# Kernel tuning notes

Hardware: AMD Instinct MI355X
Metric: run time of the kernel (lower is better)

Reference implementation:

```python
import jax, jax.numpy as jnp
import numpy as np

N_NODES = 50000
N_RAND_EDGES = 1_600_000
IN_F = 512
HID = 64
HEADS = 8
N_CLASSES = 20
SLOPE = 0.2  # LeakyReLU negative slope


def setup_inputs() -> dict:
    key = jax.random.key(0)
    ks = jax.random.split(key, 6)
    x = jax.random.normal(ks[0], (N_NODES, IN_F), dtype=jnp.float32)
    er = jax.random.randint(ks[1], (2, N_RAND_EDGES), 0, N_NODES)
    loops = jnp.tile(jnp.arange(N_NODES), (2, 1))  # self-loops so every row of adj is nonzero
    edge_index = jnp.concatenate([er, loops], axis=1)  # [2, E]
    # Learned parameters (per SpGraphAttentionLayer: weight [in,out], alpha [1,2*out] -> stored flat)
    W1 = jax.random.normal(ks[2], (HEADS, IN_F, HID), dtype=jnp.float32) * 0.05
    a1 = jax.random.normal(ks[3], (HEADS, 2 * HID), dtype=jnp.float32) * 0.1
    W2 = jax.random.normal(ks[4], (HEADS * HID, N_CLASSES), dtype=jnp.float32) * 0.05
    a2 = jax.random.normal(ks[5], (2 * N_CLASSES,), dtype=jnp.float32) * 0.1
    return {"x": x, "W1": W1, "a1": a1, "W2": W2, "a2": a2, "edge_index": edge_index}


def _gat_layer(x, W, a, e0, e1, n):
    # h = x @ weight; edge score = alpha . [h[src], h[dst]] computed as two per-node dots
    h = x @ W  # [N, F_out]
    f = W.shape[1]
    s_src = h @ a[:f]   # [N]
    s_dst = h @ a[f:]   # [N]
    edge_e = jnp.exp(jax.nn.leaky_relu(s_src[e0] + s_dst[e1], SLOPE))  # [E]
    rowsum = jax.ops.segment_sum(edge_e, e0, num_segments=n)  # spmm(adj_e, ones)
    agg = jax.ops.segment_sum(edge_e[:, None] * h[e1], e0, num_segments=n)  # spmm(adj_e, h)
    return agg / rowsum[:, None]


def reference(x, W1, a1, W2, a2, edge_index):
    n = x.shape[0]
    e0, e1 = edge_index[0], edge_index[1]
    # layer 1: per-head GAT, elu, concat along features (dropout is identity in eval)
    heads = [jax.nn.elu(_gat_layer(x, W1[i], a1[i], e0, e1, n)) for i in range(W1.shape[0])]
    hcat = jnp.concatenate(heads, axis=1)  # [N, HEADS*HID]
    out = jax.nn.elu(_gat_layer(hcat, W2, a2, e0, e1, n))  # [N, C]
    return out
```

## Files before the change

kernel.cpp:

```cpp
#include <hip/hip_runtime.h>
#include <hip/hip_fp16.h>
#include <math.h>

#define SLOPE 0.2f

typedef short bf16x8 __attribute__((ext_vector_type(8)));
typedef float f32x4  __attribute__((ext_vector_type(4)));

static __device__ __forceinline__ float elu_f(float x){ return x > 0.f ? x : (__expf(x) - 1.f); }
static __device__ __forceinline__ float lrelu(float t){ return t > 0.f ? t : SLOPE*t; }
static __device__ __forceinline__ unsigned short f2bf_rne(float f){
    unsigned int u = __float_as_uint(f);
    unsigned int r = (u + 0x7FFFu + ((u >> 16) & 1u)) >> 16;
    return (unsigned short)r;
}
static __device__ __forceinline__ float bf2f(unsigned short h){ return __uint_as_float(((unsigned int)h) << 16); }

#define ASYNC_COPY16(gp, lp) \
    __builtin_amdgcn_global_load_lds((const __attribute__((address_space(1))) void*)(gp), \
                                     (__attribute__((address_space(3))) void*)(lp), 16, 0, 0)

__global__ void __launch_bounds__(256) hist_sliced_kernel(const int* __restrict__ e0, int E, int n,
                                                          int* __restrict__ cnt){
    const int s = blockIdx.x & 7;
    const int c = blockIdx.x >> 3;
    const int K = gridDim.x >> 3;
    const int lo = (int)((long)s*n >> 3), hi = (int)((long)(s+1)*n >> 3);
    const int i0 = (int)((long)c*E/K), i1 = (int)((long)(c+1)*E/K);
    for (int i = i0 + threadIdx.x; i < i1; i += 256){
        int j = e0[i];
        if (j >= lo && j < hi) atomicAdd(&cnt[j], 1);
    }
}

__global__ void __launch_bounds__(1024) scan_kernel(const int* __restrict__ cnt, int n,
                                                    int* __restrict__ row_ptr, int* __restrict__ cursor){
    __shared__ int wtot[16];
    __shared__ int carry_sh;
    if (threadIdx.x == 0) carry_sh = 0;
    __syncthreads();
    const int lane = threadIdx.x & 63, wid = threadIdx.x >> 6;
    const int nch = (n + 1023) >> 10;
    for (int c = 0; c < nch; ++c){
        int i = (c << 10) + threadIdx.x;
        int v = (i < n) ? cnt[i] : 0;
        int val = v;
        #pragma unroll
        for (int off = 1; off < 64; off <<= 1){
            int t = __shfl_up(val, off, 64);
            if (lane >= off) val += t;
        }
        if (lane == 63) wtot[wid] = val;
        __syncthreads();
        int tot = 0, wexcl = 0;
        #pragma unroll
        for (int w = 0; w < 16; ++w){ int t = wtot[w]; tot += t; if (w < wid) wexcl += t; }
        int excl = carry_sh + wexcl + (val - v);
        if (i < n){ row_ptr[i] = excl; cursor[i] = excl; }
        __syncthreads();
        if (threadIdx.x == 0) carry_sh += tot;
        __syncthreads();
    }
    if (threadIdx.x == 0) row_ptr[n] = carry_sh;
}

__global__ void __launch_bounds__(256) scatter_sliced_kernel(const int* __restrict__ e0, const int* __restrict__ e1,
                                                             int E, int n,
                                                             int* __restrict__ cursor, int* __restrict__ sidx){
    const int s = blockIdx.x & 7;
    const int c = blockIdx.x >> 3;
    const int K = gridDim.x >> 3;
    const int lo = (int)((long)s*n >> 3), hi = (int)((long)(s+1)*n >> 3);
    const int i0 = (int)((long)c*E/K), i1 = (int)((long)(c+1)*E/K);
    for (int i = i0 + threadIdx.x; i < i1; i += 256){
        int j = e0[i];
        if (j >= lo && j < hi){
            int p = atomicAdd(&cursor[j], 1);
            sidx[p] = e1[i];
        }
    }
}

__global__ void __launch_bounds__(256) split_x_kernel(const float* __restrict__ x,
                                                      unsigned short* __restrict__ xhi,
                                                      unsigned short* __restrict__ xlo, int total4){
    int i = blockIdx.x*256 + threadIdx.x;
    if (i >= total4) return;
    float4 v = ((const float4*)x)[i];
    ushort4 h, l;
    h.x = f2bf_rne(v.x); l.x = f2bf_rne(v.x - bf2f(h.x));
    h.y = f2bf_rne(v.y); l.y = f2bf_rne(v.y - bf2f(h.y));
    h.z = f2bf_rne(v.z); l.z = f2bf_rne(v.z - bf2f(h.z));
    h.w = f2bf_rne(v.w); l.w = f2bf_rne(v.w - bf2f(h.w));
    ((ushort4*)xhi)[i] = h;
    ((ushort4*)xlo)[i] = l;
}

__global__ void __launch_bounds__(256) prep_w_kernel(const float* __restrict__ W1,
                                                     unsigned short* __restrict__ wThi,
                                                     unsigned short* __restrict__ wTlo){
    int idx = blockIdx.x*256 + threadIdx.x;
    int head = idx >> 15, rem = idx & 32767;
    int c = rem >> 9, k = rem & 511;
    float f = W1[((size_t)head << 15) + k*64 + c];
    unsigned short h = f2bf_rne(f);
    wThi[idx] = h;
    wTlo[idx] = f2bf_rne(f - bf2f(h));
}

__global__ void __launch_bounds__(256) gemm1_mfma_kernel(const unsigned short* __restrict__ xhi,
                                                         const unsigned short* __restrict__ xlo,
                                                         const unsigned short* __restrict__ wThi,
                                                         const unsigned short* __restrict__ wTlo,
                                                         const float* __restrict__ a1,
                                                         __half* __restrict__ h_g,
                                                         float* __restrict__ ssrc, float* __restrict__ sdst,
                                                         int n, int nwg){
    __shared__ unsigned short lds[16384];
    const int bid = blockIdx.x;
    const int xcd = bid & 7, jj = bid >> 3;
    const int q = nwg >> 3, r = nwg & 7;
    const int logical = (xcd < r ? xcd*(q+1) : r*(q+1) + (xcd-r)*q) + jj;
    const int rowtile = logical >> 2, ct = logical & 3;
    const int row0 = rowtile*128, col0 = ct*128;
    const int w = threadIdx.x >> 6, lane = threadIdx.x & 63;
    const int wm = w >> 1, wn = w & 1;
    const int lr = lane & 15, lk = lane >> 4;
    f32x4 acc[4][4] = {};
    const unsigned short* sbase[8];
    unsigned int soff[8];
    #pragma unroll
    for (int i = 0; i < 8; ++i){
        unsigned int off = w*8192u + i*1024u + lane*16u;
        unsigned int arr = off >> 13, within = off & 8191u;
        unsigned int rrow = within >> 6, kel = (within & 63u) >> 1;
        const unsigned short* g;
        size_t gidx;
        if (arr == 0)      { g = xhi;  gidx = (size_t)(row0 + rrow)*512 + kel; }
        else if (arr == 1) { g = xlo;  gidx = (size_t)(row0 + rrow)*512 + kel; }
        else if (arr == 2) { g = wThi; gidx = (size_t)(col0 + rrow)*512 + kel; }
        else               { g = wTlo; gidx = (size_t)(col0 + rrow)*512 + kel; }
        sbase[i] = g + gidx;
        soff[i] = (w*8192u + i*1024u);
    }
    const unsigned short* Ahi = lds;
    const unsigned short* Alo = lds + 4096;
    const unsigned short* Bhi = lds + 8192;
    const unsigned short* Blo = lds + 12288;
    for (int k0 = 0; k0 < 512; k0 += 32){
        #pragma unroll
        for (int i = 0; i < 8; ++i)
            ASYNC_COPY16(sbase[i] + k0, (char*)lds + soff[i]);
        __syncthreads();
        bf16x8 a_h[4], a_l[4], b_h[4], b_l[4];
        #pragma unroll
        for (int mi = 0; mi < 4; ++mi){
            int rowl = wm*64 + mi*16 + lr;
            a_h[mi] = *(const bf16x8*)(Ahi + rowl*32 + lk*8);
            a_l[mi] = *(const bf16x8*)(Alo + rowl*32 + lk*8);
        }
        #pragma unroll
        for (int ni = 0; ni < 4; ++ni){
            int coll = wn*64 + ni*16 + lr;
            b_h[ni] = *(const bf16x8*)(Bhi + coll*32 + lk*8);
            b_l[ni] = *(const bf16x8*)(Blo + coll*32 + lk*8);
        }
        #pragma unroll
        for (int mi = 0; mi < 4; ++mi)
            #pragma unroll
            for (int ni = 0; ni < 4; ++ni){
                f32x4& A = acc[mi][ni];
                A = __builtin_amdgcn_mfma_f32_16x16x32_bf16(a_h[mi], b_h[ni], A, 0, 0, 0);
                A = __builtin_amdgcn_mfma_f32_16x16x32_bf16(a_h[mi], b_l[ni], A, 0, 0, 0);
                A = __builtin_amdgcn_mfma_f32_16x16x32_bf16(a_l[mi], b_h[ni], A, 0, 0, 0);
            }
        __syncthreads();
    }
    const int head = ct*2 + wn;
    float as_[4], ad_[4];
    #pragma unroll
    for (int ni = 0; ni < 4; ++ni){
        as_[ni] = a1[(size_t)head*128 + ni*16 + lr];
        ad_[ni] = a1[(size_t)head*128 + 64 + ni*16 + lr];
    }
    #pragma unroll
    for (int mi = 0; mi < 4; ++mi){
        #pragma unroll
        for (int reg = 0; reg < 4; ++reg){
            float s = 0.f, d = 0.f;
            #pragma unroll
            for (int ni = 0; ni < 4; ++ni){
                float v = acc[mi][ni][reg];
                s += v*as_[ni]; d += v*ad_[ni];
            }
            s += __shfl_xor(s, 1); d += __shfl_xor(d, 1);
            s += __shfl_xor(s, 2); d += __shfl_xor(d, 2);
            s += __shfl_xor(s, 4); d += __shfl_xor(d, 4);
            s += __shfl_xor(s, 8); d += __shfl_xor(d, 8);
            const int node = row0 + wm*64 + mi*16 + lk*4 + reg;
            if (node < n){
                #pragma unroll
                for (int ni = 0; ni < 4; ++ni)
                    h_g[(size_t)node*512 + head*64 + ni*16 + lr] = __float2half(acc[mi][ni][reg]);
                if (lr == 0){
                    ssrc[(size_t)node*8 + head] = s;
                    sdst[(size_t)node*8 + head] = d;
                }
            }
        }
    }
}

__global__ void __launch_bounds__(256) agg1_kernel(const __half* __restrict__ h_g, const float* __restrict__ ssrc,
                                                   const float* __restrict__ sdst,
                                                   const int* __restrict__ row_ptr, const int* __restrict__ sidx,
                                                   __half* __restrict__ hcat, int n){
    const int w = threadIdx.x >> 6, lane = threadIdx.x & 63;
    const int node = blockIdx.x*4 + w;
    if (node >= n) return;
    const int r0 = row_ptr[node], r1 = row_ptr[node+1];
    const int h = lane >> 3;
    const float ssh = ssrc[(size_t)node*8 + h];
    float acc[8] = {};
    float wsum = 0.f;
    int e = r0;
    for (; e + 3 < r1; e += 4){
        int j0 = sidx[e], j1 = sidx[e+1], j2 = sidx[e+2], j3 = sidx[e+3];
        uint4 g0 = *(const uint4*)(h_g + (size_t)j0*512 + lane*8);
        uint4 g1 = *(const uint4*)(h_g + (size_t)j1*512 + lane*8);
        uint4 g2 = *(const uint4*)(h_g + (size_t)j2*512 + lane*8);
        uint4 g3 = *(const uint4*)(h_g + (size_t)j3*512 + lane*8);
        float s0 = sdst[(size_t)j0*8 + h], s1 = sdst[(size_t)j1*8 + h];
        float s2 = sdst[(size_t)j2*8 + h], s3 = sdst[(size_t)j3*8 + h];
        float w0 = __expf(lrelu(ssh + s0));
        float w1 = __expf(lrelu(ssh + s1));
        float w2 = __expf(lrelu(ssh + s2));
        float w3 = __expf(lrelu(ssh + s3));
        const unsigned int* u0 = &g0.x; const unsigned int* u1 = &g1.x;
        const unsigned int* u2 = &g2.x; const unsigned int* u3 = &g3.x;
        #pragma unroll
        for (int q = 0; q < 4; ++q){
            float2 f0 = __half22float2(*(const __half2*)&u0[q]);
            float2 f1 = __half22float2(*(const __half2*)&u1[q]);
            float2 f2 = __half22float2(*(const __half2*)&u2[q]);
            float2 f3 = __half22float2(*(const __half2*)&u3[q]);
            acc[2*q]   += w0*f0.x + w1*f1.x + w2*f2.x + w3*f3.x;
            acc[2*q+1] += w0*f0.y + w1*f1.y + w2*f2.y + w3*f3.y;
        }
        wsum += (w0 + w1) + (w2 + w3);
    }
    for (; e < r1; ++e){
        int j = sidx[e];
        uint4 g = *(const uint4*)(h_g + (size_t)j*512 + lane*8);
        float wg = __expf(lrelu(ssh + sdst[(size_t)j*8 + h]));
        const unsigned int* u = &g.x;
        #pragma unroll
        for (int q = 0; q < 4; ++q){
            float2 f = __half22float2(*(const __half2*)&u[q]);
            acc[2*q]   += wg*f.x;
            acc[2*q+1] += wg*f.y;
        }
        wsum += wg;
    }
    float inv = 1.f / wsum;
    union { uint4 u; __half hv[8]; } pk;
    #pragma unroll
    for (int q = 0; q < 8; ++q) pk.hv[q] = __float2half(elu_f(acc[q]*inv));
    *(uint4*)(hcat + (size_t)node*512 + lane*8) = pk.u;
}

__global__ void __launch_bounds__(256) gemm2_kernel(const __half* __restrict__ hcat, const float* __restrict__ W2,
                                                    const float* __restrict__ a2,
                                                    float* __restrict__ h2, float* __restrict__ ssrc,
                                                    float* __restrict__ sdst, int n){
    __shared__ float As[16][257];
    __shared__ float Ws[16][20];
    const int tid = threadIdx.x;
    const int node = blockIdx.x*256 + tid;
    float acc[20] = {};
    for (int k0 = 0; k0 < 512; k0 += 16){
        uint4 u0 = {0,0,0,0}, u1 = {0,0,0,0};
        if (node < n){
            const __half* src = hcat + (size_t)node*512 + k0;
            u0 = *(const uint4*)src;
            u1 = *(const uint4*)(src + 8);
        }
        const unsigned int* ua = &u0.x;
        const unsigned int* ub = &u1.x;
        #pragma unroll
        for (int q = 0; q < 4; ++q){
            float2 f = __half22float2(*(const __half2*)&ua[q]);
            As[2*q][tid] = f.x; As[2*q+1][tid] = f.y;
            float2 g = __half22float2(*(const __half2*)&ub[q]);
            As[8+2*q][tid] = g.x; As[8+2*q+1][tid] = g.y;
        }
        for (int q = tid; q < 320; q += 256){
            int kr = q/20, cc = q%20;
            Ws[kr][cc] = W2[(size_t)(k0 + kr)*20 + cc];
        }
        __syncthreads();
        #pragma unroll
        for (int kk = 0; kk < 16; ++kk){
            float a = As[kk][tid];
            #pragma unroll
            for (int cc = 0; cc < 20; ++cc) acc[cc] += a*Ws[kk][cc];
        }
        __syncthreads();
    }
    if (node < n){
        float s0 = 0.f, s1 = 0.f;
        #pragma unroll
        for (int cc = 0; cc < 20; ++cc){
            h2[(size_t)node*20 + cc] = acc[cc];
            s0 += acc[cc]*a2[cc];
            s1 += acc[cc]*a2[20 + cc];
        }
        ssrc[node] = s0; sdst[node] = s1;
    }
}

__global__ void __launch_bounds__(256) agg2_kernel(const float* __restrict__ h2, const float* __restrict__ ssrc,
                                                   const float* __restrict__ sdstv,
                                                   const int* __restrict__ row_ptr, const int* __restrict__ sidx,
                                                   float* __restrict__ out, int n){
    const int w = threadIdx.x >> 6, lane = threadIdx.x & 63;
    const int node = blockIdx.x*4 + w;
    if (node >= n) return;
    const int r0 = row_ptr[node], r1 = row_ptr[node+1];
    const float ss = ssrc[node];
    const bool act = lane < 20;
    float acc = 0.f, wsum = 0.f;
    int e = r0;
    for (; e + 3 < r1; e += 4){
        int j0 = sidx[e], j1 = sidx[e+1], j2 = sidx[e+2], j3 = sidx[e+3];
        float v0 = act ? h2[(size_t)j0*20 + lane] : 0.f;
        float v1 = act ? h2[(size_t)j1*20 + lane] : 0.f;
        float v2 = act ? h2[(size_t)j2*20 + lane] : 0.f;
        float v3 = act ? h2[(size_t)j3*20 + lane] : 0.f;
        float s0 = sdstv[j0], s1 = sdstv[j1], s2 = sdstv[j2], s3 = sdstv[j3];
        float w0 = __expf(lrelu(ss + s0));
        float w1 = __expf(lrelu(ss + s1));
        float w2 = __expf(lrelu(ss + s2));
        float w3 = __expf(lrelu(ss + s3));
        acc += w0*v0 + w1*v1 + w2*v2 + w3*v3;
        wsum += (w0 + w1) + (w2 + w3);
    }
    for (; e < r1; ++e){
        int j = sidx[e];
        float v = act ? h2[(size_t)j*20 + lane] : 0.f;
        float wg = __expf(lrelu(ss + sdstv[j]));
        acc += wg*v; wsum += wg;
    }
    if (act) out[(size_t)node*20 + lane] = elu_f(acc / wsum);
}

extern "C" void kernel_launch(void* const* d_in, const int* in_sizes, int n_in,
                              void* d_out, int out_size, void* d_ws, size_t ws_size,
                              hipStream_t stream){
    const float* x  = (const float*)d_in[0];
    const float* W1 = (const float*)d_in[1];
    const float* a1 = (const float*)d_in[2];
    const float* W2 = (const float*)d_in[3];
    const float* a2 = (const float*)d_in[4];
    const int*   ei = (const int*)d_in[5];
    const int n = in_sizes[0] / 512;
    const int E = in_sizes[5] / 2;
    const int* e0 = ei;
    const int* e1 = ei + E;

    char* p = (char*)d_ws;
    auto alloc = [&](size_t bytes)->char*{ char* r = p; p += (bytes + 255) & ~(size_t)255; return r; };
    unsigned short* xhi  = (unsigned short*)alloc((size_t)n*512*2);
    unsigned short* xlo  = (unsigned short*)alloc((size_t)n*512*2);
    __half*         h_g  = (__half*)        alloc((size_t)n*512*2);
    unsigned short* wThi = (unsigned short*)alloc((size_t)8*64*512*2);
    unsigned short* wTlo = (unsigned short*)alloc((size_t)8*64*512*2);
    float* ssrc1   = (float*)alloc((size_t)n*8*4);
    float* sdst1   = (float*)alloc((size_t)n*8*4);
    int*   cnt     = (int*)  alloc((size_t)n*4);
    int*   row_ptr = (int*)  alloc(((size_t)n + 1)*4);
    int*   cursor  = (int*)  alloc((size_t)n*4);
    int*   sidx    = (int*)  alloc((size_t)E*4);
    __half* hcat  = (__half*)xhi;
    float*  h2    = (float*)xlo;
    float*  ssrc2 = h2 + (size_t)n*20;
    float*  sdst2 = ssrc2 + n;

    hipMemsetAsync(cnt, 0, (size_t)n*4, stream);
    const int KCH = 192;
    hist_sliced_kernel   <<<KCH*8, 256, 0, stream>>>(e0, E, n, cnt);
    scan_kernel          <<<1, 1024, 0, stream>>>(cnt, n, row_ptr, cursor);
    scatter_sliced_kernel<<<KCH*8, 256, 0, stream>>>(e0, e1, E, n, cursor, sidx);

    const int total4 = n*512/4;
    split_x_kernel<<<(total4 + 255)/256, 256, 0, stream>>>(x, xhi, xlo, total4);
    prep_w_kernel <<<1024, 256, 0, stream>>>(W1, wThi, wTlo);

    const int mb = (n + 127)/128;
    const int nwg = mb*4;
    gemm1_mfma_kernel<<<nwg, 256, 0, stream>>>(xhi, xlo, wThi, wTlo, a1, h_g, ssrc1, sdst1, n, nwg);
    agg1_kernel      <<<(n + 3)/4, 256, 0, stream>>>(h_g, ssrc1, sdst1, row_ptr, sidx, hcat, n);

    const int nb256 = (n + 255)/256;
    gemm2_kernel<<<nb256, 256, 0, stream>>>(hcat, W2, a2, h2, ssrc2, sdst2, n);
    agg2_kernel <<<(n + 3)/4, 256, 0, stream>>>(h2, ssrc2, sdst2, row_ptr, sidx, (float*)d_out, n);
}
```

Baseline: 869.8 us.

## Bucket CSR neighbors by source-node range and parallelize the prefix scan

Each row's neighbor list is now grouped into buckets of 2048 source nodes by building per-(row, bucket) counters, so the aggregation gathers in agg1 and agg2 sweep through h_g in a rough, coherent order. The goal is better cache locality for the random feature gathers. The single-block serial scan is replaced by a three-kernel parallel reduce, small-scan and apply scan over the larger counter array. The CSR build now runs after gemm1, with its buffers placed inside the freed xlo workspace. In exchange, the counter array grows to n*25 entries, which adds memset, scan and atomic traffic.

```diff
diff --git a/kernel.cpp b/kernel.cpp
--- a/kernel.cpp
+++ b/kernel.cpp
@@ -3,6 +3,7 @@
 #include <math.h>
 
 #define SLOPE 0.2f
+#define SSHIFT 11
 
 typedef short bf16x8 __attribute__((ext_vector_type(8)));
 typedef float f32x4  __attribute__((ext_vector_type(4)));
@@ -20,8 +21,8 @@
     __builtin_amdgcn_global_load_lds((const __attribute__((address_space(1))) void*)(gp), \
                                      (__attribute__((address_space(3))) void*)(lp), 16, 0, 0)
 
-__global__ void __launch_bounds__(256) hist_sliced_kernel(const int* __restrict__ e0, int E, int n,
-                                                          int* __restrict__ cnt){
+__global__ void __launch_bounds__(256) hist_sliced_kernel(const int* __restrict__ e0, const int* __restrict__ e1,
+                                                          int E, int n, int NS, int* __restrict__ cnt){
     const int s = blockIdx.x & 7;
     const int c = blockIdx.x >> 3;
     const int K = gridDim.x >> 3;
@@ -29,43 +30,64 @@
     const int i0 = (int)((long)c*E/K), i1 = (int)((long)(c+1)*E/K);
     for (int i = i0 + threadIdx.x; i < i1; i += 256){
         int j = e0[i];
-        if (j >= lo && j < hi) atomicAdd(&cnt[j], 1);
-    }
-}
-
-__global__ void __launch_bounds__(1024) scan_kernel(const int* __restrict__ cnt, int n,
-                                                    int* __restrict__ row_ptr, int* __restrict__ cursor){
-    __shared__ int wtot[16];
-    __shared__ int carry_sh;
-    if (threadIdx.x == 0) carry_sh = 0;
+        if (j >= lo && j < hi) atomicAdd(&cnt[j*NS + (e1[i] >> SSHIFT)], 1);
+    }
+}
+
+__global__ void __launch_bounds__(256) scan_reduce_kernel(const int* __restrict__ cnt, int T, int* __restrict__ bsum){
+    int c0 = blockIdx.x*4096 + threadIdx.x*16;
+    int sum = 0;
+    #pragma unroll
+    for (int q = 0; q < 16; ++q){ int i = c0 + q; if (i < T) sum += cnt[i]; }
+    #pragma unroll
+    for (int off = 1; off < 64; off <<= 1) sum += __shfl_xor(sum, off, 64);
+    __shared__ int ws_[4];
+    int lane = threadIdx.x & 63, wid = threadIdx.x >> 6;
+    if (lane == 0) ws_[wid] = sum;
     __syncthreads();
-    const int lane = threadIdx.x & 63, wid = threadIdx.x >> 6;
-    const int nch = (n + 1023) >> 10;
-    for (int c = 0; c < nch; ++c){
-        int i = (c << 10) + threadIdx.x;
-        int v = (i < n) ? cnt[i] : 0;
-        int val = v;
-        #pragma unroll
-        for (int off = 1; off < 64; off <<= 1){
-            int t = __shfl_up(val, off, 64);
-            if (lane >= off) val += t;
-        }
-        if (lane == 63) wtot[wid] = val;
-        __syncthreads();
-        int tot = 0, wexcl = 0;
-        #pragma unroll
-        for (int w = 0; w < 16; ++w){ int t = wtot[w]; tot += t; if (w < wid) wexcl += t; }
-        int excl = carry_sh + wexcl + (val - v);
-        if (i < n){ row_ptr[i] = excl; cursor[i] = excl; }
-        __syncthreads();
-        if (threadIdx.x == 0) carry_sh += tot;
-        __syncthreads();
-    }
-    if (threadIdx.x == 0) row_ptr[n] = carry_sh;
+    if (threadIdx.x == 0) bsum[blockIdx.x] = ws_[0] + ws_[1] + ws_[2] + ws_[3];
+}
+
+__global__ void __launch_bounds__(512) scan_small_kernel(const int* __restrict__ bsum, int NB, int* __restrict__ bexcl){
+    int t = threadIdx.x;
+    int v = (t < NB) ? bsum[t] : 0;
+    int lane = t & 63, wid = t >> 6;
+    int val = v;
+    #pragma unroll
+    for (int off = 1; off < 64; off <<= 1){ int u = __shfl_up(val, off, 64); if (lane >= off) val += u; }
+    __shared__ int wt[8];
+    if (lane == 63) wt[wid] = val;
+    __syncthreads();
+    int base = 0;
+    for (int w2 = 0; w2 < wid; ++w2) base += wt[w2];
+    if (t < NB) bexcl[t] = base + val - v;
+}
+
+__global__ void __launch_bounds__(256) scan_apply_kernel(int* __restrict__ cnt_cur, int T,
+                                                         const int* __restrict__ bexcl){
+    int c0 = blockIdx.x*4096 + threadIdx.x*16;
+    int v[16];
+    #pragma unroll
+    for (int q = 0; q < 16; ++q){ int i = c0 + q; v[q] = (i < T) ? cnt_cur[i] : 0; }
+    int tsum = 0;
+    #pragma unroll
+    for (int q = 0; q < 16; ++q){ int t_ = v[q]; v[q] = tsum; tsum += t_; }
+    int lane = threadIdx.x & 63, wid = threadIdx.x >> 6;
+    int val = tsum;
+    #pragma unroll
+    for (int off = 1; off < 64; off <<= 1){ int u = __shfl_up(val, off, 64); if (lane >= off) val += u; }
+    __shared__ int wt[4];
+    if (lane == 63) wt[wid] = val;
+    __syncthreads();
+    int base = bexcl[blockIdx.x];
+    for (int w2 = 0; w2 < wid; ++w2) base += wt[w2];
+    base += val - tsum;
+    #pragma unroll
+    for (int q = 0; q < 16; ++q){ int i = c0 + q; if (i < T) cnt_cur[i] = base + v[q]; }
 }
 
 __global__ void __launch_bounds__(256) scatter_sliced_kernel(const int* __restrict__ e0, const int* __restrict__ e1,
-                                                             int E, int n,
+                                                             int E, int n, int NS,
                                                              int* __restrict__ cursor, int* __restrict__ sidx){
     const int s = blockIdx.x & 7;
     const int c = blockIdx.x >> 3;
@@ -75,8 +97,9 @@
     for (int i = i0 + threadIdx.x; i < i1; i += 256){
         int j = e0[i];
         if (j >= lo && j < hi){
-            int p = atomicAdd(&cursor[j], 1);
-            sidx[p] = e1[i];
+            int jj = e1[i];
+            int p = atomicAdd(&cursor[j*NS + (jj >> SSHIFT)], 1);
+            sidx[p] = jj;
         }
     }
 }
@@ -213,12 +236,13 @@
 
 __global__ void __launch_bounds__(256) agg1_kernel(const __half* __restrict__ h_g, const float* __restrict__ ssrc,
                                                    const float* __restrict__ sdst,
-                                                   const int* __restrict__ row_ptr, const int* __restrict__ sidx,
-                                                   __half* __restrict__ hcat, int n){
+                                                   const int* __restrict__ bend, const int* __restrict__ sidx,
+                                                   __half* __restrict__ hcat, int n, int NS){
     const int w = threadIdx.x >> 6, lane = threadIdx.x & 63;
     const int node = blockIdx.x*4 + w;
     if (node >= n) return;
-    const int r0 = row_ptr[node], r1 = row_ptr[node+1];
+    const int r0 = node ? bend[(size_t)node*NS - 1] : 0;
+    const int r1 = bend[(size_t)(node+1)*NS - 1];
     const int h = lane >> 3;
     const float ssh = ssrc[(size_t)node*8 + h];
     float acc[8] = {};
@@ -239,13 +263,13 @@
         const unsigned int* u0 = &g0.x; const unsigned int* u1 = &g1.x;
         const unsigned int* u2 = &g2.x; const unsigned int* u3 = &g3.x;
         #pragma unroll
-        for (int q = 0; q < 4; ++q){
-            float2 f0 = __half22float2(*(const __half2*)&u0[q]);
-            float2 f1 = __half22float2(*(const __half2*)&u1[q]);
-            float2 f2 = __half22float2(*(const __half2*)&u2[q]);
-            float2 f3 = __half22float2(*(const __half2*)&u3[q]);
-            acc[2*q]   += w0*f0.x + w1*f1.x + w2*f2.x + w3*f3.x;
-            acc[2*q+1] += w0*f0.y + w1*f1.y + w2*f2.y + w3*f3.y;
+        for (int qq = 0; qq < 4; ++qq){
+            float2 f0 = __half22float2(*(const __half2*)&u0[qq]);
+            float2 f1 = __half22float2(*(const __half2*)&u1[qq]);
+            float2 f2 = __half22float2(*(const __half2*)&u2[qq]);
+            float2 f3 = __half22float2(*(const __half2*)&u3[qq]);
+            acc[2*qq]   += w0*f0.x + w1*f1.x + w2*f2.x + w3*f3.x;
+            acc[2*qq+1] += w0*f0.y + w1*f1.y + w2*f2.y + w3*f3.y;
         }
         wsum += (w0 + w1) + (w2 + w3);
     }
@@ -255,17 +279,17 @@
         float wg = __expf(lrelu(ssh + sdst[(size_t)j*8 + h]));
         const unsigned int* u = &g.x;
         #pragma unroll
-        for (int q = 0; q < 4; ++q){
-            float2 f = __half22float2(*(const __half2*)&u[q]);
-            acc[2*q]   += wg*f.x;
-            acc[2*q+1] += wg*f.y;
+        for (int qq = 0; qq < 4; ++qq){
+            float2 f = __half22float2(*(const __half2*)&u[qq]);
+            acc[2*qq]   += wg*f.x;
+            acc[2*qq+1] += wg*f.y;
         }
         wsum += wg;
     }
     float inv = 1.f / wsum;
     union { uint4 u; __half hv[8]; } pk;
     #pragma unroll
-    for (int q = 0; q < 8; ++q) pk.hv[q] = __float2half(elu_f(acc[q]*inv));
+    for (int qq = 0; qq < 8; ++qq) pk.hv[qq] = __float2half(elu_f(acc[qq]*inv));
     *(uint4*)(hcat + (size_t)node*512 + lane*8) = pk.u;
 }
 
@@ -288,14 +312,14 @@
         const unsigned int* ua = &u0.x;
         const unsigned int* ub = &u1.x;
         #pragma unroll
-        for (int q = 0; q < 4; ++q){
-            float2 f = __half22float2(*(const __half2*)&ua[q]);
-            As[2*q][tid] = f.x; As[2*q+1][tid] = f.y;
-            float2 g = __half22float2(*(const __half2*)&ub[q]);
-            As[8+2*q][tid] = g.x; As[8+2*q+1][tid] = g.y;
-        }
-        for (int q = tid; q < 320; q += 256){
-            int kr = q/20, cc = q%20;
+        for (int qq = 0; qq < 4; ++qq){
+            float2 f = __half22float2(*(const __half2*)&ua[qq]);
+            As[2*qq][tid] = f.x; As[2*qq+1][tid] = f.y;
+            float2 g = __half22float2(*(const __half2*)&ub[qq]);
+            As[8+2*qq][tid] = g.x; As[8+2*qq+1][tid] = g.y;
+        }
+        for (int qq = tid; qq < 320; qq += 256){
+            int kr = qq/20, cc = qq%20;
             Ws[kr][cc] = W2[(size_t)(k0 + kr)*20 + cc];
         }
         __syncthreads();
@@ -321,12 +345,13 @@
 
 __global__ void __launch_bounds__(256) agg2_kernel(const float* __restrict__ h2, const float* __restrict__ ssrc,
                                                    const float* __restrict__ sdstv,
-                                                   const int* __restrict__ row_ptr, const int* __restrict__ sidx,
-                                                   float* __restrict__ out, int n){
+                                                   const int* __restrict__ bend, const int* __restrict__ sidx,
+                                                   float* __restrict__ out, int n, int NS){
     const int w = threadIdx.x >> 6, lane = threadIdx.x & 63;
     const int node = blockIdx.x*4 + w;
     if (node >= n) return;
-    const int r0 = row_ptr[node], r1 = row_ptr[node+1];
+    const int r0 = node ? bend[(size_t)node*NS - 1] : 0;
+    const int r1 = bend[(size_t)(node+1)*NS - 1];
     const float ss = ssrc[node];
     const bool act = lane < 20;
     float acc = 0.f, wsum = 0.f;
@@ -367,6 +392,8 @@
     const int E = in_sizes[5] / 2;
     const int* e0 = ei;
     const int* e1 = ei + E;
+    const int NS = (n + (1 << SSHIFT) - 1) >> SSHIFT;
+    const int T  = n * NS;
 
     char* p = (char*)d_ws;
     auto alloc = [&](size_t bytes)->char*{ char* r = p; p += (bytes + 255) & ~(size_t)255; return r; };
@@ -377,31 +404,33 @@
     unsigned short* wTlo = (unsigned short*)alloc((size_t)8*64*512*2);
     float* ssrc1   = (float*)alloc((size_t)n*8*4);
     float* sdst1   = (float*)alloc((size_t)n*8*4);
-    int*   cnt     = (int*)  alloc((size_t)n*4);
-    int*   row_ptr = (int*)  alloc(((size_t)n + 1)*4);
-    int*   cursor  = (int*)  alloc((size_t)n*4);
-    int*   sidx    = (int*)  alloc((size_t)E*4);
     __half* hcat  = (__half*)xhi;
     float*  h2    = (float*)xlo;
     float*  ssrc2 = h2 + (size_t)n*20;
     float*  sdst2 = ssrc2 + n;
-
-    hipMemsetAsync(cnt, 0, (size_t)n*4, stream);
-    const int KCH = 192;
-    hist_sliced_kernel   <<<KCH*8, 256, 0, stream>>>(e0, E, n, cnt);
-    scan_kernel          <<<1, 1024, 0, stream>>>(cnt, n, row_ptr, cursor);
-    scatter_sliced_kernel<<<KCH*8, 256, 0, stream>>>(e0, e1, E, n, cursor, sidx);
+    int*    cursor = (int*)((char*)xlo + ((size_t)6 << 20));
+    int*    sidx   = cursor + T;
+    int*    bsum   = sidx + E;
+    int*    bexcl  = bsum + 2048;
 
     const int total4 = n*512/4;
     split_x_kernel<<<(total4 + 255)/256, 256, 0, stream>>>(x, xhi, xlo, total4);
     prep_w_kernel <<<1024, 256, 0, stream>>>(W1, wThi, wTlo);
-
     const int mb = (n + 127)/128;
     const int nwg = mb*4;
     gemm1_mfma_kernel<<<nwg, 256, 0, stream>>>(xhi, xlo, wThi, wTlo, a1, h_g, ssrc1, sdst1, n, nwg);
-    agg1_kernel      <<<(n + 3)/4, 256, 0, stream>>>(h_g, ssrc1, sdst1, row_ptr, sidx, hcat, n);
-
+
+    hipMemsetAsync(cursor, 0, (size_t)T*4, stream);
+    const int KCH = 192;
+    hist_sliced_kernel<<<KCH*8, 256, 0, stream>>>(e0, e1, E, n, NS, cursor);
+    const int NB = (T + 4095)/4096;
+    scan_reduce_kernel<<<NB, 256, 0, stream>>>(cursor, T, bsum);
+    scan_small_kernel <<<1, 512, 0, stream>>>(bsum, NB, bexcl);
+    scan_apply_kernel <<<NB, 256, 0, stream>>>(cursor, T, bexcl);
+    scatter_sliced_kernel<<<KCH*8, 256, 0, stream>>>(e0, e1, E, n, NS, cursor, sidx);
+
+    agg1_kernel<<<(n + 3)/4, 256, 0, stream>>>(h_g, ssrc1, sdst1, cursor, sidx, hcat, n, NS);
     const int nb256 = (n + 255)/256;
     gemm2_kernel<<<nb256, 256, 0, stream>>>(hcat, W2, a2, h2, ssrc2, sdst2, n);
-    agg2_kernel <<<(n + 3)/4, 256, 0, stream>>>(h2, ssrc2, sdst2, row_ptr, sidx, (float*)d_out, n);
-}
+    agg2_kernel <<<(n + 3)/4, 256, 0, stream>>>(h2, ssrc2, sdst2, cursor, sidx, (float*)d_out, n, NS);
+}
```

Result: faster. 835.3 us (-4.0%).
